# Optimization experiments

Hardware: AMD Instinct MI355X
Metric: run time of the kernel (lower is better)

## Reference

```python
import jax, jax.numpy as jnp
import numpy as np
import functools, math

HEADS = 16


def _query_chunk_attention(query, key, value, precision, key_chunk_size=4096):
    # query: (q_chunk, bh, d); key/value: (kv, bh, d)
    num_kv, num_heads, k_features = key.shape[-3:]
    v_features = value.shape[-1]
    key_chunk_size = min(key_chunk_size, num_kv)
    query = query / jnp.sqrt(k_features)

    @functools.partial(jax.checkpoint, prevent_cse=False)
    def summarize_chunk(query, key, value):
        attn_weights = jnp.einsum("...qhd,...khd->...qhk", query, key, precision=precision)
        max_score = jnp.max(attn_weights, axis=-1, keepdims=True)
        max_score = jax.lax.stop_gradient(max_score)
        exp_weights = jnp.exp(attn_weights - max_score)
        exp_values = jnp.einsum("...vhf,...qhv->...qhf", value, exp_weights, precision=precision)
        max_score = jnp.einsum("...qhk->...qh", max_score)
        return exp_values, exp_weights.sum(axis=-1), max_score

    def chunk_scanner(chunk_idx):
        key_chunk = jax.lax.dynamic_slice(
            key, [chunk_idx, 0, 0], [key_chunk_size, num_heads, k_features])
        value_chunk = jax.lax.dynamic_slice(
            value, [chunk_idx, 0, 0], [key_chunk_size, num_heads, v_features])
        return summarize_chunk(query, key_chunk, value_chunk)

    chunk_values, chunk_weights, chunk_max = jax.lax.map(
        chunk_scanner, xs=jnp.arange(0, num_kv, key_chunk_size))
    # online softmax rescaling across kv chunks
    global_max = jnp.max(chunk_max, axis=0, keepdims=True)
    max_diffs = jnp.exp(chunk_max - global_max)
    chunk_values = chunk_values * jnp.expand_dims(max_diffs, axis=-1)
    chunk_weights = chunk_weights * max_diffs
    all_values = chunk_values.sum(axis=0)
    all_weights = jnp.expand_dims(chunk_weights, -1).sum(axis=0)
    return all_values / all_weights


def jax_memory_efficient_attention(query, key, value,
                                   precision=jax.lax.Precision.HIGHEST,
                                   query_chunk_size=1024, key_chunk_size=4096):
    # query: (q_len, bh, d)
    num_q, num_heads, q_features = query.shape[-3:]

    def chunk_scanner(chunk_idx, _):
        query_chunk = jax.lax.dynamic_slice(
            query, [chunk_idx, 0, 0],
            [min(query_chunk_size, num_q), num_heads, q_features])
        return (chunk_idx + query_chunk_size,
                _query_chunk_attention(query_chunk, key, value, precision, key_chunk_size))

    _, res = jax.lax.scan(chunk_scanner, 0, xs=None,
                          length=math.ceil(num_q / query_chunk_size))
    return jnp.concatenate(res, axis=-3)


def _reshape_heads_to_batch_dim(tensor, heads):
    b, s, d = tensor.shape
    t = tensor.reshape(b, s, heads, d // heads).transpose(0, 2, 1, 3)
    return t.reshape(b * heads, s, d // heads)


def _attention_fwd(query, key, value):
    heads = HEADS
    q = _reshape_heads_to_batch_dim(query, heads).transpose(1, 0, 2)  # (s, b*h, dh)
    k = _reshape_heads_to_batch_dim(key, heads).transpose(1, 0, 2)
    v = _reshape_heads_to_batch_dim(value, heads).transpose(1, 0, 2)
    flatten_latent_dim = q.shape[-3]
    if flatten_latent_dim % 64 == 0:
        query_chunk_size = flatten_latent_dim // 64
    elif flatten_latent_dim % 16 == 0:
        query_chunk_size = flatten_latent_dim // 16
    elif flatten_latent_dim % 4 == 0:
        query_chunk_size = flatten_latent_dim // 4
    else:
        query_chunk_size = flatten_latent_dim
    out = jax_memory_efficient_attention(q, k, v,
                                         query_chunk_size=query_chunk_size,
                                         key_chunk_size=4096 * 4)
    return out.transpose(1, 0, 2)  # (b*h, s, dh)


def setup_inputs() -> dict:
    key = jax.random.key(0)
    k1, k2, k3 = jax.random.split(key, 3)
    B, S, D = 2, 4096, 1024
    return {
        "query": jax.random.normal(k1, (B, S, D), dtype=jnp.float32),
        "key": jax.random.normal(k2, (B, S, D), dtype=jnp.float32),
        "value": jax.random.normal(k3, (B, S, D), dtype=jnp.float32),
    }


def reference(query, key, value):
    return _attention_fwd(query, key, value)
```

## Files before the change

kernel.cpp:

```cpp
#include <hip/hip_runtime.h>
#include <math.h>

#define SEQ    4096
#define DH     64
#define DMODEL 1024
#define NBH    32
#define NT64   64
#define LOG2E  1.44269504088896340736f

typedef __attribute__((ext_vector_type(8)))  short short8;
typedef __attribute__((ext_vector_type(4)))  float f32x4;
typedef __attribute__((ext_vector_type(16))) float f32x16;
typedef __attribute__((ext_vector_type(2)))  unsigned uint2v;

#define WS_KV_BYTES   33554432ull
#define WS_NEED_SPLIT 68157440ull

__device__ __forceinline__ unsigned short f2bf(float f) {
  union { float f; unsigned u; } x; x.f = f;
  unsigned r = x.u + 0x7FFFu + ((x.u >> 16) & 1u);
  return (unsigned short)(r >> 16);
}
__device__ __forceinline__ float bf2f(unsigned short u) {
  union { unsigned u; float f; } x; x.u = ((unsigned)u) << 16;
  return x.f;
}
__device__ __forceinline__ unsigned cvtpk_bf16(float lo, float hi) {
  unsigned r;
  asm("v_cvt_pk_bf16_f32 %0, %1, %2" : "=v"(r) : "v"(lo), "v"(hi));
  return r;
}

__global__ __launch_bounds__(256)
void prep(const float* __restrict__ Kp, const float* __restrict__ Vp,
          unsigned short* __restrict__ ws) {
  __shared__ unsigned short Kt[128 * DH];
  __shared__ unsigned short Vt[128 * DH];
  const int blk = blockIdx.x;
  const int bh = blk >> 5, t128 = blk & 31;
  const int b = bh >> 4, h = bh & 15;
  const size_t gbase = (size_t)b * SEQ * DMODEL + (size_t)h * DH +
                       (size_t)t128 * 128 * DMODEL;
  const float* Kb = Kp + gbase;
  const float* Vb = Vp + gbase;
  unsigned short* wt = ws + (size_t)bh * NT64 * 8192 + (size_t)(2 * t128) * 8192;
  const int tid = threadIdx.x;

#pragma unroll
  for (int c = 0; c < 8; ++c) {
    const int idx = c * 256 + tid;
    const int row = idx >> 4, dc = idx & 15;
    f32x4 kf = *(const f32x4*)(Kb + (size_t)row * DMODEL + dc * 4);
    f32x4 vf = *(const f32x4*)(Vb + (size_t)row * DMODEL + dc * 4);
    uint2v ku, vu;
    ku[0] = (unsigned)f2bf(kf[0]) | ((unsigned)f2bf(kf[1]) << 16);
    ku[1] = (unsigned)f2bf(kf[2]) | ((unsigned)f2bf(kf[3]) << 16);
    vu[0] = (unsigned)f2bf(vf[0]) | ((unsigned)f2bf(vf[1]) << 16);
    vu[1] = (unsigned)f2bf(vf[2]) | ((unsigned)f2bf(vf[3]) << 16);
    *(uint2v*)&Kt[row * 64 + dc * 4] = ku;
    *(uint2v*)&Vt[row * 64 + dc * 4] = vu;
  }
  __syncthreads();

#pragma unroll
  for (int c = 0; c < 4; ++c) {
    const int idx = c * 256 + tid;
    const int l31 = idx & 31, hi = (idx >> 5) & 1, d4 = (idx >> 6) & 3, kb = idx >> 8;
    const int tau = kb >> 1, kb2 = kb & 1;
    short8 v = *(const short8*)&Kt[(kb * 32 + l31) * 64 + d4 * 16 + hi * 8];
    *(short8*)&wt[tau * 8192 + (((kb2 * 4 + d4) * 2 + hi) * 32 + l31) * 8] = v;
  }
#pragma unroll
  for (int c = 0; c < 4; ++c) {
    const int idx = c * 256 + tid;
    const int l31 = idx & 31, dt = (idx >> 5) & 1, hi = (idx >> 6) & 1, k16 = idx >> 7;
    const int tau = k16 >> 2, k162 = k16 & 3;
    const int d = dt * 32 + l31, kb0 = k16 * 16 + hi * 8;
    short8 v;
#pragma unroll
    for (int j = 0; j < 8; ++j) v[j] = (short)Vt[(kb0 + j) * 64 + d];
    *(short8*)&wt[tau * 8192 + 4096 + (((k162 * 2 + hi) * 64) + dt * 32 + l31) * 8] = v;
  }
}

__device__ __forceinline__ f32x16 qk_block(const char* Lk, int kbpar, int laneK,
                                           const short8* qb, const f32x16& ZERO) {
  short8 ka0 = *(const short8*)(Lk + kbpar * 4096 + 0 * 1024 + laneK);
  short8 ka1 = *(const short8*)(Lk + kbpar * 4096 + 1 * 1024 + laneK);
  short8 ka2 = *(const short8*)(Lk + kbpar * 4096 + 2 * 1024 + laneK);
  short8 ka3 = *(const short8*)(Lk + kbpar * 4096 + 3 * 1024 + laneK);
  f32x16 z;
  __builtin_amdgcn_s_setprio(1);
  z = __builtin_amdgcn_mfma_f32_32x32x16_bf16(ka0, qb[0], ZERO, 0, 0, 0);
  z = __builtin_amdgcn_mfma_f32_32x32x16_bf16(ka1, qb[1], z, 0, 0, 0);
  z = __builtin_amdgcn_mfma_f32_32x32x16_bf16(ka2, qb[2], z, 0, 0, 0);
  z = __builtin_amdgcn_mfma_f32_32x32x16_bf16(ka3, qb[3], z, 0, 0, 0);
  __builtin_amdgcn_s_setprio(0);
  return z;
}

__device__ __forceinline__ void proc_block(f32x16& z, const char* Lv, int k16base,
                                           int laneV, f32x16& accL, f32x16& accH,
                                           float& lsum) {
#pragma unroll
  for (int r = 0; r < 16; ++r) z[r] = __builtin_amdgcn_exp2f(z[r]);
  {
    float s0 = (z[0] + z[1]) + (z[2] + z[3]);
    float s1 = (z[4] + z[5]) + (z[6] + z[7]);
    float s2 = (z[8] + z[9]) + (z[10] + z[11]);
    float s3 = (z[12] + z[13]) + (z[14] + z[15]);
    lsum += (s0 + s1) + (s2 + s3);
  }
#pragma unroll
  for (int s = 0; s < 2; ++s) {
    const int R = 8 * s;
    unsigned a0 = cvtpk_bf16(z[R + 0], z[R + 1]);
    unsigned c0 = cvtpk_bf16(z[R + 4], z[R + 5]);
    unsigned a1 = cvtpk_bf16(z[R + 2], z[R + 3]);
    unsigned c1 = cvtpk_bf16(z[R + 6], z[R + 7]);
    asm("v_permlane32_swap_b32 %0, %1" : "+v"(a0), "+v"(c0));
    asm("v_permlane32_swap_b32 %0, %1" : "+v"(a1), "+v"(c1));
    union { unsigned u[4]; short8 s8; } pw;
    pw.u[0] = a0; pw.u[1] = a1; pw.u[2] = c0; pw.u[3] = c1;
    const int k16 = k16base + s;
    short8 vb0 = *(const short8*)(Lv + k16 * 2048 + laneV);
    short8 vb1 = *(const short8*)(Lv + k16 * 2048 + 512 + laneV);
    __builtin_amdgcn_s_setprio(1);
    accL = __builtin_amdgcn_mfma_f32_32x32x16_bf16(pw.s8, vb0, accL, 0, 0, 0);
    accH = __builtin_amdgcn_mfma_f32_32x32x16_bf16(pw.s8, vb1, accH, 0, 0, 0);
    __builtin_amdgcn_s_setprio(0);
  }
}

template <bool SPLIT>
__global__ __launch_bounds__(256, 3)
void fattn(const float* __restrict__ Qp,
           const unsigned short* __restrict__ ws,
           float* __restrict__ Op) {
  __shared__ __align__(16) char lds[2][16384];

  const int tid  = threadIdx.x;
  const int lane = tid & 63;
  const int w    = tid >> 6;
  const int hi   = lane >> 5;
  const int l31  = lane & 31;

  int bh, qc, sh, rid;
  if (SPLIT) {
    const int id = blockIdx.x;
    rid = (id & 7) * 256 + (id >> 3);
    bh = rid >> 6; qc = (rid >> 1) & 31; sh = rid & 1;
  } else {
    const int id = blockIdx.x;
    rid = (id & 7) * 128 + (id >> 3);
    bh = rid >> 5; qc = rid & 31; sh = 0;
  }
  const int NTloc = SPLIT ? 32 : 64;
  const int t0    = sh * 32;
  const int q0    = qc * 128 + w * 32;

  const int b = bh >> 4, h = bh & 15;
  const float* Qb = Qp + (size_t)b * SEQ * DMODEL + (size_t)h * DH;
  const char* wsb = (const char*)(ws + (size_t)bh * NT64 * 8192);

  short8 qb[4];
  {
    const float* qr = Qb + (size_t)(q0 + l31) * DMODEL;
    const float sc = 0.125f * LOG2E;
#pragma unroll
    for (int d4 = 0; d4 < 4; ++d4) {
      const float* p = qr + d4 * 16 + hi * 8;
      f32x4 f0 = *(const f32x4*)p;
      f32x4 f1 = *(const f32x4*)(p + 4);
      short8 v;
#pragma unroll
      for (int i = 0; i < 4; ++i) {
        v[i]     = (short)f2bf(f0[i] * sc);
        v[i + 4] = (short)f2bf(f1[i] * sc);
      }
      qb[d4] = v;
    }
  }

  f32x16 ZERO;
#pragma unroll
  for (int r = 0; r < 16; ++r) ZERO[r] = 0.f;
  f32x16 accL = ZERO, accH = ZERO;
  float lsum = 0.f;

  const int laneK = hi * 512 + l31 * 16;
  const int laneV = hi * 1024 + l31 * 16;

#define STAGE(buf_, tau_)                                                     \
  {                                                                           \
    const char* src_ = wsb + (size_t)(tau_) * 16384;                          \
    char* dst_ = &lds[buf_][0];                                               \
    _Pragma("unroll")                                                         \
    for (int c_ = 0; c_ < 4; ++c_) {                                          \
      __builtin_amdgcn_global_load_lds(                                       \
          (const __attribute__((address_space(1))) void*)(src_ + c_ * 4096 +  \
                                                          tid * 16),          \
          (__attribute__((address_space(3))) void*)(dst_ + c_ * 4096 +        \
                                                    tid * 16),                \
          16, 0, 0);                                                          \
    }                                                                         \
  }

  STAGE(0, t0);
  __syncthreads();

  f32x16 zE, zO;
  for (int t = 0; t < NTloc; ++t) {
    const int cur = t & 1;
    const char* Lk  = &lds[cur][0];
    const char* Lv  = &lds[cur][8192];
    const char* LvO = &lds[cur ^ 1][8192];

    zE = qk_block(Lk, 0, laneK, qb, ZERO);
    if (t > 0)
      proc_block(zO, LvO, 2, laneV, accL, accH, lsum);
    __syncthreads();
    if (t + 1 < NTloc) STAGE(cur ^ 1, t0 + t + 1);
    zO = qk_block(Lk, 1, laneK, qb, ZERO);
    proc_block(zE, Lv, 0, laneV, accL, accH, lsum);
    __syncthreads();
  }
  proc_block(zO, &lds[(NTloc - 1) & 1][8192], 2, laneV, accL, accH, lsum);

  if (SPLIT) {
    unsigned short* part =
        (unsigned short*)((char*)(unsigned short*)const_cast<unsigned short*>(ws) +
                          WS_KV_BYTES) + (size_t)rid * 8192;
    float* lout = (float*)((char*)const_cast<unsigned short*>(ws) +
                           2 * WS_KV_BYTES) + (size_t)rid * 128;
    const float lt = lsum + __shfl_xor(lsum, 32, 64);
    if (hi == 0) lout[w * 32 + l31] = lt;
#pragma unroll
    for (int r = 0; r < 16; ++r) {
      const int qrow = (r & 3) + 8 * (r >> 2) + 4 * hi;
      part[(w * 32 + qrow) * 64 + l31]      = f2bf(accL[r]);
      part[(w * 32 + qrow) * 64 + 32 + l31] = f2bf(accH[r]);
    }
  } else {
    const float lt  = lsum + __shfl_xor(lsum, 32, 64);
    const float inv = 1.0f / lt;
#pragma unroll
    for (int r = 0; r < 16; ++r) {
      const int qrow = (r & 3) + 8 * (r >> 2) + 4 * hi;
      const float iv = __shfl(inv, qrow + (lane & 32), 64);
      const size_t row = (size_t)bh * SEQ + q0 + qrow;
      Op[row * DH + l31]      = accL[r] * iv;
      Op[row * DH + 32 + l31] = accH[r] * iv;
    }
  }
#undef STAGE
}

__global__ __launch_bounds__(256)
void combine(const unsigned short* __restrict__ ws, float* __restrict__ Op) {
  const unsigned short* part = (const unsigned short*)((const char*)ws + WS_KV_BYTES);
  const float* lsum = (const float*)((const char*)ws + 2 * WS_KV_BYTES);
  const int gid = blockIdx.x * 256 + threadIdx.x;
  const int bqc = gid >> 10;
  const int rem = gid & 1023;
  const int q = rem >> 3, dc = rem & 7;
  const int pid0 = bqc * 2, pid1 = pid0 + 1;
  short8 A0 = *(const short8*)&part[(size_t)pid0 * 8192 + q * 64 + dc * 8];
  short8 A1 = *(const short8*)&part[(size_t)pid1 * 8192 + q * 64 + dc * 8];
  const float l = lsum[pid0 * 128 + q] + lsum[pid1 * 128 + q];
  const float inv = 1.0f / l;
  const int bh = bqc >> 5, qc = bqc & 31;
  float* o = Op + ((size_t)bh * SEQ + qc * 128 + q) * DH + dc * 8;
  f32x4 o0, o1;
#pragma unroll
  for (int j = 0; j < 4; ++j) {
    o0[j] = (bf2f((unsigned short)A0[j]) + bf2f((unsigned short)A1[j])) * inv;
    o1[j] = (bf2f((unsigned short)A0[j + 4]) + bf2f((unsigned short)A1[j + 4])) * inv;
  }
  *(f32x4*)o = o0;
  *(f32x4*)(o + 4) = o1;
}

extern "C" void kernel_launch(void* const* d_in, const int* in_sizes, int n_in,
                              void* d_out, int out_size, void* d_ws, size_t ws_size,
                              hipStream_t stream) {
  const float* Q = (const float*)d_in[0];
  const float* K = (const float*)d_in[1];
  const float* V = (const float*)d_in[2];
  float* O = (float*)d_out;
  unsigned short* ws = (unsigned short*)d_ws;

  prep<<<dim3(NBH * 32), dim3(256), 0, stream>>>(K, V, ws);
  if (ws_size >= WS_NEED_SPLIT) {
    fattn<true><<<dim3(2048), dim3(256), 0, stream>>>(Q, ws, O);
    combine<<<dim3(4096), dim3(256), 0, stream>>>(ws, O);
  } else {
    fattn<false><<<dim3(1024), dim3(256), 0, stream>>>(Q, ws, O);
  }
}
```

Before: 170.3 us.

## Prefetch odd-half V fragments into registers and drop one barrier per tile

The odd half's V fragments are loaded from LDS into registers in the same iteration as the QK products, and processed in the next iteration. The other LDS buffer is then no longer read after the iteration ends. This lets the next tile's async global-to-LDS stage start at the top of the loop, and the mid-loop __syncthreads is removed, leaving one barrier per tile. The intent is to cut barrier stalls and overlap the copy with more compute. The cost is extra live VGPRs for the held V fragments, which could pressure occupancy under the 3-blocks-per-CU launch bound.

```diff
diff --git a/kernel.cpp b/kernel.cpp
--- a/kernel.cpp
+++ b/kernel.cpp
@@ -99,9 +99,11 @@
   return z;
 }
 
-__device__ __forceinline__ void proc_block(f32x16& z, const char* Lv, int k16base,
-                                           int laneV, f32x16& accL, f32x16& accH,
-                                           float& lsum) {
+__device__ __forceinline__ void proc_core(f32x16& z,
+                                          short8 v0a, short8 v0b,
+                                          short8 v1a, short8 v1b,
+                                          f32x16& accL, f32x16& accH,
+                                          float& lsum) {
 #pragma unroll
   for (int r = 0; r < 16; ++r) z[r] = __builtin_amdgcn_exp2f(z[r]);
   {
@@ -122,12 +124,14 @@
     asm("v_permlane32_swap_b32 %0, %1" : "+v"(a1), "+v"(c1));
     union { unsigned u[4]; short8 s8; } pw;
     pw.u[0] = a0; pw.u[1] = a1; pw.u[2] = c0; pw.u[3] = c1;
-    const int k16 = k16base + s;
-    short8 vb0 = *(const short8*)(Lv + k16 * 2048 + laneV);
-    short8 vb1 = *(const short8*)(Lv + k16 * 2048 + 512 + laneV);
     __builtin_amdgcn_s_setprio(1);
-    accL = __builtin_amdgcn_mfma_f32_32x32x16_bf16(pw.s8, vb0, accL, 0, 0, 0);
-    accH = __builtin_amdgcn_mfma_f32_32x32x16_bf16(pw.s8, vb1, accH, 0, 0, 0);
+    if (s == 0) {
+      accL = __builtin_amdgcn_mfma_f32_32x32x16_bf16(pw.s8, v0a, accL, 0, 0, 0);
+      accH = __builtin_amdgcn_mfma_f32_32x32x16_bf16(pw.s8, v0b, accH, 0, 0, 0);
+    } else {
+      accL = __builtin_amdgcn_mfma_f32_32x32x16_bf16(pw.s8, v1a, accL, 0, 0, 0);
+      accH = __builtin_amdgcn_mfma_f32_32x32x16_bf16(pw.s8, v1b, accH, 0, 0, 0);
+    }
     __builtin_amdgcn_s_setprio(0);
   }
 }
@@ -209,28 +213,40 @@
   STAGE(0, t0);
   __syncthreads();
 
-  f32x16 zE, zO;
+  f32x16 zO;
+  short8 vO0a, vO0b, vO1a, vO1b;
+
   for (int t = 0; t < NTloc; ++t) {
     const int cur = t & 1;
-    const char* Lk  = &lds[cur][0];
-    const char* Lv  = &lds[cur][8192];
-    const char* LvO = &lds[cur ^ 1][8192];
-
-    zE = qk_block(Lk, 0, laneK, qb, ZERO);
+    const char* Lk = &lds[cur][0];
+    const char* Lv = &lds[cur][8192];
+
+    if (t + 1 < NTloc) STAGE(cur ^ 1, t0 + t + 1);
+
+    f32x16 zE = qk_block(Lk, 0, laneK, qb, ZERO);
     if (t > 0)
-      proc_block(zO, LvO, 2, laneV, accL, accH, lsum);
+      proc_core(zO, vO0a, vO0b, vO1a, vO1b, accL, accH, lsum);
+
+    zO = qk_block(Lk, 1, laneK, qb, ZERO);
+    vO0a = *(const short8*)(Lv + 2 * 2048 + laneV);
+    vO0b = *(const short8*)(Lv + 2 * 2048 + 512 + laneV);
+    vO1a = *(const short8*)(Lv + 3 * 2048 + laneV);
+    vO1b = *(const short8*)(Lv + 3 * 2048 + 512 + laneV);
+
+    short8 e0a = *(const short8*)(Lv + 0 * 2048 + laneV);
+    short8 e0b = *(const short8*)(Lv + 0 * 2048 + 512 + laneV);
+    short8 e1a = *(const short8*)(Lv + 1 * 2048 + laneV);
+    short8 e1b = *(const short8*)(Lv + 1 * 2048 + 512 + laneV);
+    proc_core(zE, e0a, e0b, e1a, e1b, accL, accH, lsum);
+
     __syncthreads();
-    if (t + 1 < NTloc) STAGE(cur ^ 1, t0 + t + 1);
-    zO = qk_block(Lk, 1, laneK, qb, ZERO);
-    proc_block(zE, Lv, 0, laneV, accL, accH, lsum);
-    __syncthreads();
-  }
-  proc_block(zO, &lds[(NTloc - 1) & 1][8192], 2, laneV, accL, accH, lsum);
+  }
+  proc_core(zO, vO0a, vO0b, vO1a, vO1b, accL, accH, lsum);
 
   if (SPLIT) {
     unsigned short* part =
-        (unsigned short*)((char*)(unsigned short*)const_cast<unsigned short*>(ws) +
-                          WS_KV_BYTES) + (size_t)rid * 8192;
+        (unsigned short*)((char*)const_cast<unsigned short*>(ws) + WS_KV_BYTES) +
+        (size_t)rid * 8192;
     float* lout = (float*)((char*)const_cast<unsigned short*>(ws) +
                            2 * WS_KV_BYTES) + (size_t)rid * 128;
     const float lt = lsum + __shfl_xor(lsum, 32, 64);
```

After: 173.1 us. Within noise of the previous version (+1.7%).
